# Kernel tuning notes

Hardware: AMD Instinct MI355X
Metric: run time of the kernel (lower is better)

## Reference

```python
import jax, jax.numpy as jnp
import numpy as np

N, E, D, H, C, G = 80000, 1280000, 64, 64, 5, 512


def setup_inputs() -> dict:
    key = jax.random.key(0)
    ks = jax.random.split(key, 8)
    h = jax.random.normal(ks[0], (N, D), jnp.float32)
    src = jax.random.randint(ks[1], (E,), 0, N)
    dst = jax.random.randint(ks[2], (E,), 0, N)
    graph_ids = jnp.sort(jax.random.randint(ks[3], (N,), 0, G))
    # Glorot-ish init for weights
    W1 = jax.random.normal(ks[4], (D, H), jnp.float32) * (1.0 / np.sqrt(D))
    b1 = jnp.zeros((H,), jnp.float32)
    W2 = jax.random.normal(ks[5], (H, H), jnp.float32) * (1.0 / np.sqrt(H))
    b2 = jnp.zeros((H,), jnp.float32)
    Wc = jax.random.normal(ks[6], (H, C), jnp.float32) * (1.0 / np.sqrt(H))
    bc = jnp.zeros((C,), jnp.float32)
    return dict(h=h, src=src, dst=dst, graph_ids=graph_ids,
                W1=W1, b1=b1, W2=W2, b2=b2, Wc=Wc, bc=bc, num_graphs=G)


def reference(h, src, dst, graph_ids, W1, b1, W2, b2, Wc, bc, num_graphs):
    n = h.shape[0]
    ones_e = jnp.ones(src.shape[0], h.dtype)
    # DGL GraphConv norm='both': symmetric normalization, degrees clamped to >=1
    out_deg = jnp.clip(jax.ops.segment_sum(ones_e, src, num_segments=n), 1.0)
    in_deg = jnp.clip(jax.ops.segment_sum(ones_e, dst, num_segments=n), 1.0)
    norm_src = jax.lax.rsqrt(out_deg)  # [N]
    norm_dst = jax.lax.rsqrt(in_deg)   # [N]

    def graph_conv(x, W, b):
        x = x * norm_src[:, None]                                   # scale by D_out^{-1/2}
        agg = jax.ops.segment_sum(x[src], dst, num_segments=n)      # sparse A^T x (copy_u + sum)
        agg = agg * norm_dst[:, None]                               # scale by D_in^{-1/2}
        return agg @ W + b

    h1 = jax.nn.relu(graph_conv(h, W1, b1))
    h2 = jax.nn.relu(graph_conv(h1, W2, b2))

    # dgl.mean_nodes: per-graph mean pooling over nodes
    cnt = jnp.clip(jax.ops.segment_sum(jnp.ones(n, h.dtype), graph_ids,
                                       num_segments=num_graphs), 1.0)
    hg = jax.ops.segment_sum(h2, graph_ids, num_segments=num_graphs) / cnt[:, None]
    return hg @ Wc + bc  # [G, C] logits
```

## Files before the change

kernel.cpp:

```cpp
#include <hip/hip_runtime.h>
#include <hip/hip_bf16.h>


#define NBK 160
#define HB  256
#define CAP 9216

typedef __attribute__((ext_vector_type(8))) short bf16x8;
typedef __attribute__((ext_vector_type(4))) float f32x4;

__device__ __forceinline__ float bflo(unsigned u) { return __uint_as_float(u << 16); }
__device__ __forceinline__ float bfhi(unsigned u) { return __uint_as_float(u & 0xffff0000u); }
__device__ __forceinline__ float bf1(unsigned short u) { return __uint_as_float((unsigned)u << 16); }
__device__ __forceinline__ unsigned short f2bf(float f) {
    unsigned u = __float_as_uint(f);
    return (unsigned short)((u + 0x7fff + ((u >> 16) & 1)) >> 16);
}
__device__ __forceinline__ unsigned packbf(float lo, float hi) {
    return (unsigned)f2bf(lo) | ((unsigned)f2bf(hi) << 16);
}

__global__ __launch_bounds__(256) void pA_scatter(
    const int* __restrict__ src, const int* __restrict__ dst,
    int* __restrict__ curD, int* __restrict__ curS,
    int* __restrict__ pack, unsigned short* __restrict__ sloc,
    const int* __restrict__ gids, int* __restrict__ goffs,
    int E, int NB, int N, int G)
{
    if (blockIdx.x >= HB) {
        int i = (blockIdx.x - HB) * 256 + threadIdx.x;
        if (i >= N) return;
        int b = gids[i];
        if (i == 0) {
            for (int g = 0; g <= b; g++) goffs[g] = 0;
        } else {
            int a = gids[i - 1];
            for (int g = a + 1; g <= b; g++) goffs[g] = i;
        }
        if (i == N - 1) {
            for (int g = b + 1; g <= G; g++) goffs[g] = N;
        }
        return;
    }
    __shared__ int hd[NBK], hs[NBK];
    int t = threadIdx.x;
    for (int i = t; i < NB; i += 256) { hd[i] = 0; hs[i] = 0; }
    __syncthreads();
    int chunk = (E + HB - 1) / HB;
    int s0 = blockIdx.x * chunk, s1 = min(E, s0 + chunk);
    int q0 = s0 >> 2, q1 = s1 >> 2;
    const int4* s4 = (const int4*)src;
    const int4* d4 = (const int4*)dst;
    for (int q = q0 + t; q < q1; q += 256) {
        int4 d = d4[q];
        int4 s = s4[q];
        atomicAdd(&hd[d.x >> 9], 1); atomicAdd(&hd[d.y >> 9], 1);
        atomicAdd(&hd[d.z >> 9], 1); atomicAdd(&hd[d.w >> 9], 1);
        atomicAdd(&hs[s.x >> 9], 1); atomicAdd(&hs[s.y >> 9], 1);
        atomicAdd(&hs[s.z >> 9], 1); atomicAdd(&hs[s.w >> 9], 1);
    }
    for (int i = (q1 << 2) + t; i < s1; i += 256) {
        atomicAdd(&hd[dst[i] >> 9], 1);
        atomicAdd(&hs[src[i] >> 9], 1);
    }
    __syncthreads();
    for (int b = t; b < NB; b += 256) {
        int cd = hd[b], cs = hs[b];
        hd[b] = cd ? atomicAdd(&curD[b], cd) : 0;
        hs[b] = cs ? atomicAdd(&curS[b], cs) : 0;
    }
    __syncthreads();
    for (int q = q0 + t; q < q1; q += 256) {
        int4 d = d4[q];
        int4 s = s4[q];
        #pragma unroll
        for (int j = 0; j < 4; j++) {
            int ss = j == 0 ? s.x : j == 1 ? s.y : j == 2 ? s.z : s.w;
            int dd = j == 0 ? d.x : j == 1 ? d.y : j == 2 ? d.z : d.w;
            int bd = dd >> 9, bs = ss >> 9;
            int pd = atomicAdd(&hd[bd], 1);
            int ps = atomicAdd(&hs[bs], 1);
            if (pd < CAP) pack[(size_t)bd * CAP + pd] = ((dd & 511) << 17) | ss;
            if (ps < CAP) sloc[(size_t)bs * CAP + ps] = (unsigned short)(ss & 511);
        }
    }
    for (int i = (q1 << 2) + t; i < s1; i += 256) {
        int s = src[i], d = dst[i];
        int bd = d >> 9, bs = s >> 9;
        int pd = atomicAdd(&hd[bd], 1);
        int ps = atomicAdd(&hs[bs], 1);
        if (pd < CAP) pack[(size_t)bd * CAP + pd] = ((d & 511) << 17) | s;
        if (ps < CAP) sloc[(size_t)bs * CAP + ps] = (unsigned short)(s & 511);
    }
}

__global__ __launch_bounds__(256) void p5_build(
    const int* __restrict__ pack, const unsigned short* __restrict__ sloc,
    const int* __restrict__ curD, const int* __restrict__ curS,
    int* __restrict__ col, int* __restrict__ row_offs, int* __restrict__ deg,
    float* __restrict__ nsrc, float* __restrict__ ndst,
    const float* __restrict__ h, unsigned short* __restrict__ xs,
    int N, int NB)
{
    __shared__ int hist[512];
    __shared__ float nsl[512];
    __shared__ int wt[4];
    int t = threadIdx.x;
    bool dmode = blockIdx.x < NB;
    int b = dmode ? blockIdx.x : blockIdx.x - NB;
    int n0 = b << 9, n1 = min(N, n0 + 512);
    hist[t] = 0; hist[t + 256] = 0;
    __syncthreads();
    int e0 = b * CAP;
    int tot = min(dmode ? curD[b] : curS[b], CAP);
    int e1 = e0 + tot;
    if (!dmode) {
        for (int i = e0 + t; i < e1; i += 256)
            atomicAdd(&hist[sloc[i]], 1);
        __syncthreads();
        for (int n = n0 + t; n < n1; n += 256) {
            float s = rsqrtf((float)max(hist[n - n0], 1));
            nsrc[n] = s;
            nsl[n - n0] = s;
        }
        __syncthreads();
        int cnt = n1 - n0;
        const float2* h2p = (const float2*)h;
        ushort2* xp = (ushort2*)xs;
        for (int i = t; i < cnt * 32; i += 256) {
            int node = i >> 5;
            float s = nsl[node];
            float2 v = h2p[(size_t)(n0 + node) * 32 + (i & 31)];
            ushort2 o;
            o.x = f2bf(v.x * s);
            o.y = f2bf(v.y * s);
            xp[(size_t)(n0 + node) * 32 + (i & 31)] = o;
        }
        return;
    }
    for (int i = e0 + t; i < e1; i += 256)
        atomicAdd(&hist[pack[i] >> 17], 1);
    __syncthreads();
    int c0 = hist[2 * t], c1 = hist[2 * t + 1];
    int v = c0 + c1;
    int lane = t & 63, w = t >> 6;
    int x = v;
    #pragma unroll
    for (int off = 1; off < 64; off <<= 1) {
        int y = __shfl_up(x, off);
        if (lane >= off) x += y;
    }
    if (lane == 63) wt[w] = x;
    __syncthreads();
    int bw = 0;
    for (int i = 0; i < w; i++) bw += wt[i];
    int excl = x - v + bw;
    int n = n0 + 2 * t;
    if (n < n1) {
        row_offs[n] = e0 + excl;
        deg[n] = c0;
        ndst[n] = rsqrtf((float)max(c0, 1));
    }
    if (n + 1 < n1) {
        row_offs[n + 1] = e0 + excl + c0;
        deg[n + 1] = c1;
        ndst[n + 1] = rsqrtf((float)max(c1, 1));
    }
    hist[2 * t] = excl;
    hist[2 * t + 1] = excl + c0;
    __syncthreads();
    for (int i = e0 + t; i < e1; i += 256) {
        int wd = pack[i];
        int pos = atomicAdd(&hist[wd >> 17], 1);
        col[e0 + pos] = wd & 0x1FFFF;
    }
}

__global__ __launch_bounds__(256) void agg_kernel(
    const unsigned short* __restrict__ z, unsigned short* __restrict__ y,
    const int* __restrict__ col, const int* __restrict__ row_offs,
    const int* __restrict__ deg, int N)
{
    int lane = threadIdx.x & 63;
    int sub  = lane >> 3;
    int li   = lane & 7;
    const uint4* x4 = (const uint4*)z;

    int wid = (blockIdx.x * 256 + threadIdx.x) >> 6;
    int nw  = (gridDim.x * 256) >> 6;

    int ro = 0, cnt = 0, idx = 0;
    if (wid < N) {
        ro = row_offs[wid];
        cnt = deg[wid];
        if (lane < min(cnt, 64)) idx = col[ro + lane];
    }
    for (int node = wid; node < N; node += nw) {
        int nnode = node + nw;
        int nro = 0, ncnt = 0;
        if (nnode < N) { nro = row_offs[nnode]; ncnt = deg[nnode]; }

        float a0=0.f,a1=0.f,a2=0.f,a3=0.f,a4=0.f,a5=0.f,a6=0.f,a7=0.f;
        int cc = 0;
        int cidx = idx;
        while (cc < cnt) {
            int m = min(cnt - cc, 64);
            for (int i = 0; i < m; i += 32) {
                int e1 = i + sub, e2 = i + 8 + sub, e3 = i + 16 + sub, e4 = i + 24 + sub;
                int s1 = __shfl(cidx, min(e1, m - 1));
                int s2 = __shfl(cidx, min(e2, m - 1));
                int s3 = __shfl(cidx, min(e3, m - 1));
                int s4 = __shfl(cidx, min(e4, m - 1));
                uint4 v1 = make_uint4(0u,0u,0u,0u), v2 = v1, v3 = v1, v4 = v1;
                if (e1 < m) v1 = x4[(size_t)s1 * 8 + li];
                if (e2 < m) v2 = x4[(size_t)s2 * 8 + li];
                if (e3 < m) v3 = x4[(size_t)s3 * 8 + li];
                if (e4 < m) v4 = x4[(size_t)s4 * 8 + li];
                a0 += bflo(v1.x); a1 += bfhi(v1.x);
                a2 += bflo(v1.y); a3 += bfhi(v1.y);
                a4 += bflo(v1.z); a5 += bfhi(v1.z);
                a6 += bflo(v1.w); a7 += bfhi(v1.w);
                a0 += bflo(v2.x); a1 += bfhi(v2.x);
                a2 += bflo(v2.y); a3 += bfhi(v2.y);
                a4 += bflo(v2.z); a5 += bfhi(v2.z);
                a6 += bflo(v2.w); a7 += bfhi(v2.w);
                a0 += bflo(v3.x); a1 += bfhi(v3.x);
                a2 += bflo(v3.y); a3 += bfhi(v3.y);
                a4 += bflo(v3.z); a5 += bfhi(v3.z);
                a6 += bflo(v3.w); a7 += bfhi(v3.w);
                a0 += bflo(v4.x); a1 += bfhi(v4.x);
                a2 += bflo(v4.y); a3 += bfhi(v4.y);
                a4 += bflo(v4.z); a5 += bfhi(v4.z);
                a6 += bflo(v4.w); a7 += bfhi(v4.w);
            }
            cc += 64;
            if (cc < cnt) cidx = (lane < min(cnt - cc, 64)) ? col[ro + cc + lane] : 0;
        }
        idx = 0;
        if (nnode < N && lane < min(ncnt, 64)) idx = col[nro + lane];

        #pragma unroll
        for (int off = 8; off <= 32; off <<= 1) {
            a0 += __shfl_xor(a0, off); a1 += __shfl_xor(a1, off);
            a2 += __shfl_xor(a2, off); a3 += __shfl_xor(a3, off);
            a4 += __shfl_xor(a4, off); a5 += __shfl_xor(a5, off);
            a6 += __shfl_xor(a6, off); a7 += __shfl_xor(a7, off);
        }
        if (sub == 0) {
            uint4 o;
            o.x = packbf(a0, a1);
            o.y = packbf(a2, a3);
            o.z = packbf(a4, a5);
            o.w = packbf(a6, a7);
            ((uint4*)y)[(size_t)node * 8 + li] = o;
        }
        ro = nro; cnt = ncnt;
    }
}

__global__ __launch_bounds__(256) void gemm_kernel(
    const unsigned short* __restrict__ A, const float* __restrict__ W,
    const float* __restrict__ b, const float* __restrict__ ndst,
    const float* __restrict__ nsrc, unsigned short* __restrict__ Z,
    int M, int scale_out)
{
    int t = threadIdx.x, lane = t & 63, w = t >> 6;
    int col = lane & 15, quad = lane >> 4;
    bf16x8 bfrag[4][2];
    #pragma unroll
    for (int nt = 0; nt < 4; nt++)
        #pragma unroll
        for (int ks = 0; ks < 2; ks++)
            #pragma unroll
            for (int j = 0; j < 8; j++)
                bfrag[nt][ks][j] =
                    (short)f2bf(W[(ks * 32 + quad * 8 + j) * 64 + nt * 16 + col]);
    float bias[4];
    #pragma unroll
    for (int nt = 0; nt < 4; nt++) bias[nt] = b[nt * 16 + col];

    int mbase = blockIdx.x * 64 + w * 16;
    if (mbase >= M) return;
    int row = min(mbase + col, M - 1);
    const uint4* a4 = (const uint4*)A;
    union { uint4 u; bf16x8 v; } a0, a1;
    a0.u = a4[(size_t)row * 8 + quad];
    a1.u = a4[(size_t)row * 8 + 4 + quad];

    float nd[4], ns[4];
    #pragma unroll
    for (int r = 0; r < 4; r++) {
        int m = min(mbase + quad * 4 + r, M - 1);
        nd[r] = ndst[m];
        ns[r] = scale_out ? nsrc[m] : 1.f;
    }

    #pragma unroll
    for (int nt = 0; nt < 4; nt++) {
        f32x4 acc = {0.f, 0.f, 0.f, 0.f};
        acc = __builtin_amdgcn_mfma_f32_16x16x32_bf16(a0.v, bfrag[nt][0], acc, 0, 0, 0);
        acc = __builtin_amdgcn_mfma_f32_16x16x32_bf16(a1.v, bfrag[nt][1], acc, 0, 0, 0);
        #pragma unroll
        for (int r = 0; r < 4; r++) {
            int m = mbase + quad * 4 + r;
            if (m < M)
                Z[(size_t)m * 64 + nt * 16 + col] =
                    f2bf(fmaxf(nd[r] * acc[r] + bias[nt], 0.f) * ns[r]);
        }
    }
}

__global__ __launch_bounds__(256) void pool_kernel(
    const unsigned short* __restrict__ h2, const int* __restrict__ goffs,
    const float* __restrict__ Wc, const float* __restrict__ bc,
    float* __restrict__ out)
{
    int g = blockIdx.x;
    int lane = threadIdx.x & 63;
    int w = threadIdx.x >> 6;
    int s = goffs[g], e = goffs[g + 1];
    float acc = 0.f;
    for (int i = s + w; i < e; i += 4) acc += bf1(h2[i * 64 + lane]);
    __shared__ float red[4][64];
    red[w][lane] = acc;
    __syncthreads();
    if (w == 0) {
        float tot = red[0][lane] + red[1][lane] + red[2][lane] + red[3][lane];
        float mean = tot / (float)max(e - s, 1);
        float wc[5];
        #pragma unroll
        for (int c = 0; c < 5; c++) wc[c] = Wc[lane * 5 + c];
        #pragma unroll
        for (int c = 0; c < 5; c++) {
            float p = mean * wc[c];
            #pragma unroll
            for (int off = 32; off; off >>= 1) p += __shfl_down(p, off);
            if (lane == 0) out[g * 5 + c] = p + bc[c];
        }
    }
}

extern "C" void kernel_launch(void* const* d_in, const int* in_sizes, int n_in,
                              void* d_out, int out_size, void* d_ws, size_t ws_size,
                              hipStream_t stream)
{
    const float* h    = (const float*)d_in[0];
    const int*   src  = (const int*)d_in[1];
    const int*   dst  = (const int*)d_in[2];
    const int*   gids = (const int*)d_in[3];
    const float* W1   = (const float*)d_in[4];
    const float* b1   = (const float*)d_in[5];
    const float* W2   = (const float*)d_in[6];
    const float* b2   = (const float*)d_in[7];
    const float* Wc   = (const float*)d_in[8];
    const float* bc   = (const float*)d_in[9];
    float* out = (float*)d_out;

    const int N = in_sizes[0] / 64;
    const int E = in_sizes[1];
    const int G = out_size / 5;
    const int NB = (N + 511) >> 9;
    const int NBB = (N + 255) / 256;

    auto align = [](size_t x) { return (x + 255) & ~(size_t)255; };
    char* p = (char*)d_ws;
    int* curD    = (int*)p;            p += align((size_t)2 * NBK * 4);
    int* curS    = curD + NBK;
    int* row_offs= (int*)p;            p += align((size_t)N * 4);
    int* deg     = (int*)p;            p += align((size_t)N * 4);
    float* nsrc  = (float*)p;          p += align((size_t)N * 4);
    float* ndst  = (float*)p;          p += align((size_t)N * 4);
    int* goffs   = (int*)p;            p += align((size_t)(G + 1) * 4);
    int* pack    = (int*)p;            p += align((size_t)NBK * CAP * 4);
    unsigned short* sloc = (unsigned short*)p; p += align((size_t)NBK * CAP * 2);
    int* col     = (int*)p;            p += align((size_t)NBK * CAP * 4);
    unsigned short* xs  = (unsigned short*)p; p += align((size_t)N * 64 * 2);
    unsigned short* s1  = (unsigned short*)p; p += align((size_t)N * 64 * 2);
    unsigned short* h1s = (unsigned short*)p; p += align((size_t)N * 64 * 2);
    unsigned short* s2  = s1;
    unsigned short* h2  = xs;

    hipMemsetAsync(curD, 0, (size_t)2 * NBK * 4, stream);

    pA_scatter<<<HB + NBB, 256, 0, stream>>>(src, dst, curD, curS, pack, sloc,
                                             gids, goffs, E, NB, N, G);
    p5_build<<<2 * NB, 256, 0, stream>>>(pack, sloc, curD, curS, col,
                                         row_offs, deg, nsrc, ndst, h, xs, N, NB);

    agg_kernel<<<4096, 256, 0, stream>>>(xs, s1, col, row_offs, deg, N);
    gemm_kernel<<<(N + 63) / 64, 256, 0, stream>>>(s1, W1, b1, ndst, nsrc,
                                                   h1s, N, 1);
    agg_kernel<<<4096, 256, 0, stream>>>(h1s, s2, col, row_offs, deg, N);
    gemm_kernel<<<(N + 63) / 64, 256, 0, stream>>>(s2, W2, b2, ndst, nsrc,
                                                   h2, N, 0);

    pool_kernel<<<G, 256, 0, stream>>>(h2, goffs, Wc, bc, out);
}
```

Measured before the change: 224.4 us.

## Fuse all seven kernels into one cooperative persistent kernel with grid syncs

Replaces the sequence of scatter, CSR build, two aggregation, two GEMM and pooling launches with a single cooperative kernel. The phases are separated by grid-wide syncs and use grid-stride loops over virtual blocks. This removes per-launch overhead and inter-kernel gaps. In exchange the grid is capped at the occupancy limit, which may reduce parallelism for agg (previously 4096 blocks) and adds grid-barrier cost.

```diff
diff --git a/kernel.cpp b/kernel.cpp
--- a/kernel.cpp
+++ b/kernel.cpp
@@ -1,5 +1,8 @@
 #include <hip/hip_runtime.h>
 #include <hip/hip_bf16.h>
+#include <hip/hip_cooperative_groups.h>
+
+namespace cg = cooperative_groups;
 
 
 #define NBK 160
@@ -20,171 +23,15 @@
     return (unsigned)f2bf(lo) | ((unsigned)f2bf(hi) << 16);
 }
 
-__global__ __launch_bounds__(256) void pA_scatter(
-    const int* __restrict__ src, const int* __restrict__ dst,
-    int* __restrict__ curD, int* __restrict__ curS,
-    int* __restrict__ pack, unsigned short* __restrict__ sloc,
-    const int* __restrict__ gids, int* __restrict__ goffs,
-    int E, int NB, int N, int G)
-{
-    if (blockIdx.x >= HB) {
-        int i = (blockIdx.x - HB) * 256 + threadIdx.x;
-        if (i >= N) return;
-        int b = gids[i];
-        if (i == 0) {
-            for (int g = 0; g <= b; g++) goffs[g] = 0;
-        } else {
-            int a = gids[i - 1];
-            for (int g = a + 1; g <= b; g++) goffs[g] = i;
-        }
-        if (i == N - 1) {
-            for (int g = b + 1; g <= G; g++) goffs[g] = N;
-        }
-        return;
-    }
-    __shared__ int hd[NBK], hs[NBK];
-    int t = threadIdx.x;
-    for (int i = t; i < NB; i += 256) { hd[i] = 0; hs[i] = 0; }
-    __syncthreads();
-    int chunk = (E + HB - 1) / HB;
-    int s0 = blockIdx.x * chunk, s1 = min(E, s0 + chunk);
-    int q0 = s0 >> 2, q1 = s1 >> 2;
-    const int4* s4 = (const int4*)src;
-    const int4* d4 = (const int4*)dst;
-    for (int q = q0 + t; q < q1; q += 256) {
-        int4 d = d4[q];
-        int4 s = s4[q];
-        atomicAdd(&hd[d.x >> 9], 1); atomicAdd(&hd[d.y >> 9], 1);
-        atomicAdd(&hd[d.z >> 9], 1); atomicAdd(&hd[d.w >> 9], 1);
-        atomicAdd(&hs[s.x >> 9], 1); atomicAdd(&hs[s.y >> 9], 1);
-        atomicAdd(&hs[s.z >> 9], 1); atomicAdd(&hs[s.w >> 9], 1);
-    }
-    for (int i = (q1 << 2) + t; i < s1; i += 256) {
-        atomicAdd(&hd[dst[i] >> 9], 1);
-        atomicAdd(&hs[src[i] >> 9], 1);
-    }
-    __syncthreads();
-    for (int b = t; b < NB; b += 256) {
-        int cd = hd[b], cs = hs[b];
-        hd[b] = cd ? atomicAdd(&curD[b], cd) : 0;
-        hs[b] = cs ? atomicAdd(&curS[b], cs) : 0;
-    }
-    __syncthreads();
-    for (int q = q0 + t; q < q1; q += 256) {
-        int4 d = d4[q];
-        int4 s = s4[q];
-        #pragma unroll
-        for (int j = 0; j < 4; j++) {
-            int ss = j == 0 ? s.x : j == 1 ? s.y : j == 2 ? s.z : s.w;
-            int dd = j == 0 ? d.x : j == 1 ? d.y : j == 2 ? d.z : d.w;
-            int bd = dd >> 9, bs = ss >> 9;
-            int pd = atomicAdd(&hd[bd], 1);
-            int ps = atomicAdd(&hs[bs], 1);
-            if (pd < CAP) pack[(size_t)bd * CAP + pd] = ((dd & 511) << 17) | ss;
-            if (ps < CAP) sloc[(size_t)bs * CAP + ps] = (unsigned short)(ss & 511);
-        }
-    }
-    for (int i = (q1 << 2) + t; i < s1; i += 256) {
-        int s = src[i], d = dst[i];
-        int bd = d >> 9, bs = s >> 9;
-        int pd = atomicAdd(&hd[bd], 1);
-        int ps = atomicAdd(&hs[bs], 1);
-        if (pd < CAP) pack[(size_t)bd * CAP + pd] = ((d & 511) << 17) | s;
-        if (ps < CAP) sloc[(size_t)bs * CAP + ps] = (unsigned short)(s & 511);
-    }
-}
-
-__global__ __launch_bounds__(256) void p5_build(
-    const int* __restrict__ pack, const unsigned short* __restrict__ sloc,
-    const int* __restrict__ curD, const int* __restrict__ curS,
-    int* __restrict__ col, int* __restrict__ row_offs, int* __restrict__ deg,
-    float* __restrict__ nsrc, float* __restrict__ ndst,
-    const float* __restrict__ h, unsigned short* __restrict__ xs,
-    int N, int NB)
-{
-    __shared__ int hist[512];
-    __shared__ float nsl[512];
-    __shared__ int wt[4];
-    int t = threadIdx.x;
-    bool dmode = blockIdx.x < NB;
-    int b = dmode ? blockIdx.x : blockIdx.x - NB;
-    int n0 = b << 9, n1 = min(N, n0 + 512);
-    hist[t] = 0; hist[t + 256] = 0;
-    __syncthreads();
-    int e0 = b * CAP;
-    int tot = min(dmode ? curD[b] : curS[b], CAP);
-    int e1 = e0 + tot;
-    if (!dmode) {
-        for (int i = e0 + t; i < e1; i += 256)
-            atomicAdd(&hist[sloc[i]], 1);
-        __syncthreads();
-        for (int n = n0 + t; n < n1; n += 256) {
-            float s = rsqrtf((float)max(hist[n - n0], 1));
-            nsrc[n] = s;
-            nsl[n - n0] = s;
-        }
-        __syncthreads();
-        int cnt = n1 - n0;
-        const float2* h2p = (const float2*)h;
-        ushort2* xp = (ushort2*)xs;
-        for (int i = t; i < cnt * 32; i += 256) {
-            int node = i >> 5;
-            float s = nsl[node];
-            float2 v = h2p[(size_t)(n0 + node) * 32 + (i & 31)];
-            ushort2 o;
-            o.x = f2bf(v.x * s);
-            o.y = f2bf(v.y * s);
-            xp[(size_t)(n0 + node) * 32 + (i & 31)] = o;
-        }
-        return;
-    }
-    for (int i = e0 + t; i < e1; i += 256)
-        atomicAdd(&hist[pack[i] >> 17], 1);
-    __syncthreads();
-    int c0 = hist[2 * t], c1 = hist[2 * t + 1];
-    int v = c0 + c1;
-    int lane = t & 63, w = t >> 6;
-    int x = v;
-    #pragma unroll
-    for (int off = 1; off < 64; off <<= 1) {
-        int y = __shfl_up(x, off);
-        if (lane >= off) x += y;
-    }
-    if (lane == 63) wt[w] = x;
-    __syncthreads();
-    int bw = 0;
-    for (int i = 0; i < w; i++) bw += wt[i];
-    int excl = x - v + bw;
-    int n = n0 + 2 * t;
-    if (n < n1) {
-        row_offs[n] = e0 + excl;
-        deg[n] = c0;
-        ndst[n] = rsqrtf((float)max(c0, 1));
-    }
-    if (n + 1 < n1) {
-        row_offs[n + 1] = e0 + excl + c0;
-        deg[n + 1] = c1;
-        ndst[n + 1] = rsqrtf((float)max(c1, 1));
-    }
-    hist[2 * t] = excl;
-    hist[2 * t + 1] = excl + c0;
-    __syncthreads();
-    for (int i = e0 + t; i < e1; i += 256) {
-        int wd = pack[i];
-        int pos = atomicAdd(&hist[wd >> 17], 1);
-        col[e0 + pos] = wd & 0x1FFFF;
-    }
-}
-
-__global__ __launch_bounds__(256) void agg_kernel(
-    const unsigned short* __restrict__ z, unsigned short* __restrict__ y,
-    const int* __restrict__ col, const int* __restrict__ row_offs,
+__device__ __forceinline__ void agg_body(
+    const unsigned short* __restrict__ zin, unsigned short* __restrict__ yout,
+    const int* __restrict__ cols, const int* __restrict__ row_offs,
     const int* __restrict__ deg, int N)
 {
     int lane = threadIdx.x & 63;
     int sub  = lane >> 3;
     int li   = lane & 7;
-    const uint4* x4 = (const uint4*)z;
+    const uint4* x4 = (const uint4*)zin;
 
     int wid = (blockIdx.x * 256 + threadIdx.x) >> 6;
     int nw  = (gridDim.x * 256) >> 6;
@@ -193,7 +40,7 @@
     if (wid < N) {
         ro = row_offs[wid];
         cnt = deg[wid];
-        if (lane < min(cnt, 64)) idx = col[ro + lane];
+        if (lane < min(cnt, 64)) idx = cols[ro + lane];
     }
     for (int node = wid; node < N; node += nw) {
         int nnode = node + nw;
@@ -234,10 +81,10 @@
                 a6 += bflo(v4.w); a7 += bfhi(v4.w);
             }
             cc += 64;
-            if (cc < cnt) cidx = (lane < min(cnt - cc, 64)) ? col[ro + cc + lane] : 0;
+            if (cc < cnt) cidx = (lane < min(cnt - cc, 64)) ? cols[ro + cc + lane] : 0;
         }
         idx = 0;
-        if (nnode < N && lane < min(ncnt, 64)) idx = col[nro + lane];
+        if (nnode < N && lane < min(ncnt, 64)) idx = cols[nro + lane];
 
         #pragma unroll
         for (int off = 8; off <= 32; off <<= 1) {
@@ -252,20 +99,20 @@
             o.y = packbf(a2, a3);
             o.z = packbf(a4, a5);
             o.w = packbf(a6, a7);
-            ((uint4*)y)[(size_t)node * 8 + li] = o;
+            ((uint4*)yout)[(size_t)node * 8 + li] = o;
         }
         ro = nro; cnt = ncnt;
     }
 }
 
-__global__ __launch_bounds__(256) void gemm_kernel(
+__device__ __forceinline__ void gemm_body(
     const unsigned short* __restrict__ A, const float* __restrict__ W,
-    const float* __restrict__ b, const float* __restrict__ ndst,
+    const float* __restrict__ bb, const float* __restrict__ ndst,
     const float* __restrict__ nsrc, unsigned short* __restrict__ Z,
     int M, int scale_out)
 {
-    int t = threadIdx.x, lane = t & 63, w = t >> 6;
-    int col = lane & 15, quad = lane >> 4;
+    int t = threadIdx.x, lane = t & 63, w4 = t >> 6;
+    int cl = lane & 15, quad = lane >> 4;
     bf16x8 bfrag[4][2];
     #pragma unroll
     for (int nt = 0; nt < 4; nt++)
@@ -274,69 +121,246 @@
             #pragma unroll
             for (int j = 0; j < 8; j++)
                 bfrag[nt][ks][j] =
-                    (short)f2bf(W[(ks * 32 + quad * 8 + j) * 64 + nt * 16 + col]);
+                    (short)f2bf(W[(ks * 32 + quad * 8 + j) * 64 + nt * 16 + cl]);
     float bias[4];
     #pragma unroll
-    for (int nt = 0; nt < 4; nt++) bias[nt] = b[nt * 16 + col];
-
-    int mbase = blockIdx.x * 64 + w * 16;
-    if (mbase >= M) return;
-    int row = min(mbase + col, M - 1);
-    const uint4* a4 = (const uint4*)A;
-    union { uint4 u; bf16x8 v; } a0, a1;
-    a0.u = a4[(size_t)row * 8 + quad];
-    a1.u = a4[(size_t)row * 8 + 4 + quad];
-
-    float nd[4], ns[4];
-    #pragma unroll
-    for (int r = 0; r < 4; r++) {
-        int m = min(mbase + quad * 4 + r, M - 1);
-        nd[r] = ndst[m];
-        ns[r] = scale_out ? nsrc[m] : 1.f;
-    }
-
-    #pragma unroll
-    for (int nt = 0; nt < 4; nt++) {
-        f32x4 acc = {0.f, 0.f, 0.f, 0.f};
-        acc = __builtin_amdgcn_mfma_f32_16x16x32_bf16(a0.v, bfrag[nt][0], acc, 0, 0, 0);
-        acc = __builtin_amdgcn_mfma_f32_16x16x32_bf16(a1.v, bfrag[nt][1], acc, 0, 0, 0);
+    for (int nt = 0; nt < 4; nt++) bias[nt] = bb[nt * 16 + cl];
+
+    int ntiles = (M + 63) >> 6;
+    for (int tb = blockIdx.x; tb < ntiles; tb += gridDim.x) {
+        int mbase = tb * 64 + w4 * 16;
+        if (mbase >= M) continue;
+        int row = min(mbase + cl, M - 1);
+        const uint4* a4 = (const uint4*)A;
+        union { uint4 u; bf16x8 v; } a0, a1;
+        a0.u = a4[(size_t)row * 8 + quad];
+        a1.u = a4[(size_t)row * 8 + 4 + quad];
+
+        float nd[4], ns[4];
         #pragma unroll
         for (int r = 0; r < 4; r++) {
-            int m = mbase + quad * 4 + r;
-            if (m < M)
-                Z[(size_t)m * 64 + nt * 16 + col] =
-                    f2bf(fmaxf(nd[r] * acc[r] + bias[nt], 0.f) * ns[r]);
-        }
-    }
-}
-
-__global__ __launch_bounds__(256) void pool_kernel(
-    const unsigned short* __restrict__ h2, const int* __restrict__ goffs,
+            int m = min(mbase + quad * 4 + r, M - 1);
+            nd[r] = ndst[m];
+            ns[r] = scale_out ? nsrc[m] : 1.f;
+        }
+
+        #pragma unroll
+        for (int nt = 0; nt < 4; nt++) {
+            f32x4 acc = {0.f, 0.f, 0.f, 0.f};
+            acc = __builtin_amdgcn_mfma_f32_16x16x32_bf16(a0.v, bfrag[nt][0], acc, 0, 0, 0);
+            acc = __builtin_amdgcn_mfma_f32_16x16x32_bf16(a1.v, bfrag[nt][1], acc, 0, 0, 0);
+            #pragma unroll
+            for (int r = 0; r < 4; r++) {
+                int m = mbase + quad * 4 + r;
+                if (m < M)
+                    Z[(size_t)m * 64 + nt * 16 + cl] =
+                        f2bf(fmaxf(nd[r] * acc[r] + bias[nt], 0.f) * ns[r]);
+            }
+        }
+    }
+}
+
+__global__ __launch_bounds__(256, 4) void fused_all(
+    const float* __restrict__ h, const int* __restrict__ src,
+    const int* __restrict__ dst, const int* __restrict__ gids,
+    const float* __restrict__ W1, const float* __restrict__ b1,
+    const float* __restrict__ W2, const float* __restrict__ b2,
     const float* __restrict__ Wc, const float* __restrict__ bc,
-    float* __restrict__ out)
+    float* __restrict__ out,
+    int* curD, int* curS, int* row_offs, int* deg,
+    float* nsrc, float* ndst, int* goffs, int* pack,
+    unsigned short* sloc, int* cols,
+    unsigned short* xs, unsigned short* sb1, unsigned short* h1s,
+    int N, int E, int G, int NB)
 {
-    int g = blockIdx.x;
-    int lane = threadIdx.x & 63;
-    int w = threadIdx.x >> 6;
-    int s = goffs[g], e = goffs[g + 1];
-    float acc = 0.f;
-    for (int i = s + w; i < e; i += 4) acc += bf1(h2[i * 64 + lane]);
-    __shared__ float red[4][64];
-    red[w][lane] = acc;
-    __syncthreads();
-    if (w == 0) {
-        float tot = red[0][lane] + red[1][lane] + red[2][lane] + red[3][lane];
-        float mean = tot / (float)max(e - s, 1);
-        float wc[5];
-        #pragma unroll
-        for (int c = 0; c < 5; c++) wc[c] = Wc[lane * 5 + c];
-        #pragma unroll
-        for (int c = 0; c < 5; c++) {
-            float p = mean * wc[c];
+    cg::grid_group gg = cg::this_grid();
+    __shared__ int smem[1040];
+    const int t = threadIdx.x;
+    const int NBB = (N + 255) >> 8;
+
+    for (int vb = blockIdx.x; vb < HB + NBB; vb += gridDim.x) {
+        if (vb >= HB) {
+            int i = (vb - HB) * 256 + t;
+            if (i < N) {
+                int b = gids[i];
+                if (i == 0) {
+                    for (int g = 0; g <= b; g++) goffs[g] = 0;
+                } else {
+                    int a = gids[i - 1];
+                    for (int g = a + 1; g <= b; g++) goffs[g] = i;
+                }
+                if (i == N - 1) {
+                    for (int g = b + 1; g <= G; g++) goffs[g] = N;
+                }
+            }
+        } else {
+            int* hd = smem;
+            int* hs = smem + NBK;
+            for (int i = t; i < NB; i += 256) { hd[i] = 0; hs[i] = 0; }
+            __syncthreads();
+            int chunk = (E + HB - 1) / HB;
+            int s0 = vb * chunk, se = min(E, s0 + chunk);
+            int q0 = s0 >> 2, q1 = se >> 2;
+            const int4* s4 = (const int4*)src;
+            const int4* d4 = (const int4*)dst;
+            for (int q = q0 + t; q < q1; q += 256) {
+                int4 d = d4[q];
+                int4 s = s4[q];
+                atomicAdd(&hd[d.x >> 9], 1); atomicAdd(&hd[d.y >> 9], 1);
+                atomicAdd(&hd[d.z >> 9], 1); atomicAdd(&hd[d.w >> 9], 1);
+                atomicAdd(&hs[s.x >> 9], 1); atomicAdd(&hs[s.y >> 9], 1);
+                atomicAdd(&hs[s.z >> 9], 1); atomicAdd(&hs[s.w >> 9], 1);
+            }
+            for (int i = (q1 << 2) + t; i < se; i += 256) {
+                atomicAdd(&hd[dst[i] >> 9], 1);
+                atomicAdd(&hs[src[i] >> 9], 1);
+            }
+            __syncthreads();
+            for (int b = t; b < NB; b += 256) {
+                int cd = hd[b], cs = hs[b];
+                hd[b] = cd ? atomicAdd(&curD[b], cd) : 0;
+                hs[b] = cs ? atomicAdd(&curS[b], cs) : 0;
+            }
+            __syncthreads();
+            for (int q = q0 + t; q < q1; q += 256) {
+                int4 d = d4[q];
+                int4 s = s4[q];
+                #pragma unroll
+                for (int j = 0; j < 4; j++) {
+                    int ss = j == 0 ? s.x : j == 1 ? s.y : j == 2 ? s.z : s.w;
+                    int dd = j == 0 ? d.x : j == 1 ? d.y : j == 2 ? d.z : d.w;
+                    int bd = dd >> 9, bs = ss >> 9;
+                    int pd = atomicAdd(&hd[bd], 1);
+                    int ps = atomicAdd(&hs[bs], 1);
+                    if (pd < CAP) pack[(size_t)bd * CAP + pd] = ((dd & 511) << 17) | ss;
+                    if (ps < CAP) sloc[(size_t)bs * CAP + ps] = (unsigned short)(ss & 511);
+                }
+            }
+            for (int i = (q1 << 2) + t; i < se; i += 256) {
+                int s = src[i], d = dst[i];
+                int bd = d >> 9, bs = s >> 9;
+                int pd = atomicAdd(&hd[bd], 1);
+                int ps = atomicAdd(&hs[bs], 1);
+                if (pd < CAP) pack[(size_t)bd * CAP + pd] = ((d & 511) << 17) | s;
+                if (ps < CAP) sloc[(size_t)bs * CAP + ps] = (unsigned short)(s & 511);
+            }
+            __syncthreads();
+        }
+    }
+    gg.sync();
+
+    for (int vb = blockIdx.x; vb < 2 * NB; vb += gridDim.x) {
+        int* hist = smem;
+        float* nsl = (float*)(smem + 512);
+        int* wt = smem + 1024;
+        bool dmode = vb < NB;
+        int b = dmode ? vb : vb - NB;
+        int n0 = b << 9, n1 = min(N, n0 + 512);
+        hist[t] = 0; hist[t + 256] = 0;
+        __syncthreads();
+        int e0 = b * CAP;
+        int tot = min(dmode ? curD[b] : curS[b], CAP);
+        int e1 = e0 + tot;
+        if (!dmode) {
+            for (int i = e0 + t; i < e1; i += 256)
+                atomicAdd(&hist[sloc[i]], 1);
+            __syncthreads();
+            for (int n = n0 + t; n < n1; n += 256) {
+                float sc = rsqrtf((float)max(hist[n - n0], 1));
+                nsrc[n] = sc;
+                nsl[n - n0] = sc;
+            }
+            __syncthreads();
+            int cnt = n1 - n0;
+            const float2* h2p = (const float2*)h;
+            ushort2* xp = (ushort2*)xs;
+            for (int i = t; i < cnt * 32; i += 256) {
+                int node = i >> 5;
+                float sc = nsl[node];
+                float2 v = h2p[(size_t)(n0 + node) * 32 + (i & 31)];
+                ushort2 o;
+                o.x = f2bf(v.x * sc);
+                o.y = f2bf(v.y * sc);
+                xp[(size_t)(n0 + node) * 32 + (i & 31)] = o;
+            }
+        } else {
+            for (int i = e0 + t; i < e1; i += 256)
+                atomicAdd(&hist[pack[i] >> 17], 1);
+            __syncthreads();
+            int c0 = hist[2 * t], c1 = hist[2 * t + 1];
+            int v = c0 + c1;
+            int lane = t & 63, w4 = t >> 6;
+            int x = v;
             #pragma unroll
-            for (int off = 32; off; off >>= 1) p += __shfl_down(p, off);
-            if (lane == 0) out[g * 5 + c] = p + bc[c];
-        }
+            for (int off = 1; off < 64; off <<= 1) {
+                int y = __shfl_up(x, off);
+                if (lane >= off) x += y;
+            }
+            if (lane == 63) wt[w4] = x;
+            __syncthreads();
+            int bw = 0;
+            for (int i = 0; i < w4; i++) bw += wt[i];
+            int excl = x - v + bw;
+            int n = n0 + 2 * t;
+            if (n < n1) {
+                row_offs[n] = e0 + excl;
+                deg[n] = c0;
+                ndst[n] = rsqrtf((float)max(c0, 1));
+            }
+            if (n + 1 < n1) {
+                row_offs[n + 1] = e0 + excl + c0;
+                deg[n + 1] = c1;
+                ndst[n + 1] = rsqrtf((float)max(c1, 1));
+            }
+            hist[2 * t] = excl;
+            hist[2 * t + 1] = excl + c0;
+            __syncthreads();
+            for (int i = e0 + t; i < e1; i += 256) {
+                int wd = pack[i];
+                int pos = atomicAdd(&hist[wd >> 17], 1);
+                cols[e0 + pos] = wd & 0x1FFFF;
+            }
+        }
+        __syncthreads();
+    }
+    gg.sync();
+
+    agg_body(xs, sb1, cols, row_offs, deg, N);
+    gg.sync();
+    gemm_body(sb1, W1, b1, ndst, nsrc, h1s, N, 1);
+    gg.sync();
+
+    agg_body(h1s, sb1, cols, row_offs, deg, N);
+    gg.sync();
+    gemm_body(sb1, W2, b2, ndst, nsrc, xs, N, 0);
+    gg.sync();
+
+    const unsigned short* h2 = xs;
+    for (int g = blockIdx.x; g < G; g += gridDim.x) {
+        int lane = t & 63;
+        int w4 = t >> 6;
+        int s = goffs[g], e = goffs[g + 1];
+        float acc = 0.f;
+        for (int i = s + w4; i < e; i += 4) acc += bf1(h2[(size_t)i * 64 + lane]);
+        float* red = (float*)smem;
+        red[w4 * 64 + lane] = acc;
+        __syncthreads();
+        if (w4 == 0) {
+            float tot = red[0 * 64 + lane] + red[1 * 64 + lane] +
+                        red[2 * 64 + lane] + red[3 * 64 + lane];
+            float mean = tot / (float)max(e - s, 1);
+            float wc[5];
+            #pragma unroll
+            for (int c = 0; c < 5; c++) wc[c] = Wc[lane * 5 + c];
+            #pragma unroll
+            for (int c = 0; c < 5; c++) {
+                float p = mean * wc[c];
+                #pragma unroll
+                for (int off = 32; off; off >>= 1) p += __shfl_down(p, off);
+                if (lane == 0) out[g * 5 + c] = p + bc[c];
+            }
+        }
+        __syncthreads();
     }
 }
 
@@ -356,11 +380,10 @@
     const float* bc   = (const float*)d_in[9];
     float* out = (float*)d_out;
 
-    const int N = in_sizes[0] / 64;
-    const int E = in_sizes[1];
-    const int G = out_size / 5;
-    const int NB = (N + 511) >> 9;
-    const int NBB = (N + 255) / 256;
+    int N = in_sizes[0] / 64;
+    int E = in_sizes[1];
+    int G = out_size / 5;
+    int NB = (N + 511) >> 9;
 
     auto align = [](size_t x) { return (x + 255) & ~(size_t)255; };
     char* p = (char*)d_ws;
@@ -373,26 +396,26 @@
     int* goffs   = (int*)p;            p += align((size_t)(G + 1) * 4);
     int* pack    = (int*)p;            p += align((size_t)NBK * CAP * 4);
     unsigned short* sloc = (unsigned short*)p; p += align((size_t)NBK * CAP * 2);
-    int* col     = (int*)p;            p += align((size_t)NBK * CAP * 4);
+    int* cols    = (int*)p;            p += align((size_t)NBK * CAP * 4);
     unsigned short* xs  = (unsigned short*)p; p += align((size_t)N * 64 * 2);
-    unsigned short* s1  = (unsigned short*)p; p += align((size_t)N * 64 * 2);
+    unsigned short* sb1 = (unsigned short*)p; p += align((size_t)N * 64 * 2);
     unsigned short* h1s = (unsigned short*)p; p += align((size_t)N * 64 * 2);
-    unsigned short* s2  = s1;
-    unsigned short* h2  = xs;
+
+    static int grid_blocks = 0;
+    if (grid_blocks == 0) {
+        int perCU = 0;
+        if (hipOccupancyMaxActiveBlocksPerMultiprocessor(&perCU, fused_all, 256, 0)
+                != hipSuccess || perCU < 1)
+            perCU = 2;
+        grid_blocks = perCU * 256;
+        if (grid_blocks > 2048) grid_blocks = 2048;
+    }
 
     hipMemsetAsync(curD, 0, (size_t)2 * NBK * 4, stream);
 
-    pA_scatter<<<HB + NBB, 256, 0, stream>>>(src, dst, curD, curS, pack, sloc,
-                                             gids, goffs, E, NB, N, G);
-    p5_build<<<2 * NB, 256, 0, stream>>>(pack, sloc, curD, curS, col,
-                                         row_offs, deg, nsrc, ndst, h, xs, N, NB);
-
-    agg_kernel<<<4096, 256, 0, stream>>>(xs, s1, col, row_offs, deg, N);
-    gemm_kernel<<<(N + 63) / 64, 256, 0, stream>>>(s1, W1, b1, ndst, nsrc,
-                                                   h1s, N, 1);
-    agg_kernel<<<4096, 256, 0, stream>>>(h1s, s2, col, row_offs, deg, N);
-    gemm_kernel<<<(N + 63) / 64, 256, 0, stream>>>(s2, W2, b2, ndst, nsrc,
-                                                   h2, N, 0);
-
-    pool_kernel<<<G, 256, 0, stream>>>(h2, goffs, Wc, bc, out);
-}
+    void* args[] = { &h, &src, &dst, &gids, &W1, &b1, &W2, &b2, &Wc, &bc, &out,
+                     &curD, &curS, &row_offs, &deg, &nsrc, &ndst, &goffs, &pack,
+                     &sloc, &cols, &xs, &sb1, &h1s, &N, &E, &G, &NB };
+    hipLaunchCooperativeKernel((void*)fused_all, dim3(grid_blocks), dim3(256),
+                               args, 0, stream);
+}
```

Measured after the change: 655.4 us. 2.92x slower.

## Fuse aggregation with dense transform and pooling into per-node GEMV kernels

Applied to the files above, without the earlier changes.

Each layer's aggregation kernel now multiplies the aggregated row by the weight matrix directly, using a per-wave scalar GEMV with W kept in shared memory, instead of writing an intermediate and running a separate MFMA GEMM kernel. The second layer accumulates its output straight into per-graph sums with atomics, which removes the h2 write and the pool read. The goal is to drop two kernel launches and the intermediate activation traffic. The cost is 64 FMAs plus 64 shuffles per node on CUDA cores instead of MFMA, a 16KB shared-memory load of W per block, and float atomic contention on graph accumulators.

```diff
diff --git a/kernel.cpp b/kernel.cpp
--- a/kernel.cpp
+++ b/kernel.cpp
@@ -15,9 +15,6 @@
 __device__ __forceinline__ unsigned short f2bf(float f) {
     unsigned u = __float_as_uint(f);
     return (unsigned short)((u + 0x7fff + ((u >> 16) & 1)) >> 16);
-}
-__device__ __forceinline__ unsigned packbf(float lo, float hi) {
-    return (unsigned)f2bf(lo) | ((unsigned)f2bf(hi) << 16);
 }
 
 __global__ __launch_bounds__(256) void pA_scatter(
@@ -176,15 +173,24 @@
     }
 }
 
-__global__ __launch_bounds__(256) void agg_kernel(
-    const unsigned short* __restrict__ z, unsigned short* __restrict__ y,
-    const int* __restrict__ col, const int* __restrict__ row_offs,
-    const int* __restrict__ deg, int N)
-{
+template<int MODE>
+__global__ __launch_bounds__(256) void agg_gemv(
+    const unsigned short* __restrict__ zin, unsigned short* __restrict__ yout,
+    const int* __restrict__ cols, const int* __restrict__ row_offs,
+    const int* __restrict__ deg, const float* __restrict__ W,
+    const float* __restrict__ bias, const float* __restrict__ ndst,
+    const float* __restrict__ nsrc, const int* __restrict__ gids,
+    float* __restrict__ gacc, int N)
+{
+    __shared__ float Wl[4096];
+    for (int i = threadIdx.x; i < 4096; i += 256) Wl[i] = W[i];
+    __syncthreads();
+
     int lane = threadIdx.x & 63;
     int sub  = lane >> 3;
     int li   = lane & 7;
-    const uint4* x4 = (const uint4*)z;
+    float bv = bias[lane];
+    const uint4* x4 = (const uint4*)zin;
 
     int wid = (blockIdx.x * 256 + threadIdx.x) >> 6;
     int nw  = (gridDim.x * 256) >> 6;
@@ -193,14 +199,14 @@
     if (wid < N) {
         ro = row_offs[wid];
         cnt = deg[wid];
-        if (lane < min(cnt, 64)) idx = col[ro + lane];
+        if (lane < min(cnt, 64)) idx = cols[ro + lane];
     }
     for (int node = wid; node < N; node += nw) {
         int nnode = node + nw;
         int nro = 0, ncnt = 0;
         if (nnode < N) { nro = row_offs[nnode]; ncnt = deg[nnode]; }
 
-        float a0=0.f,a1=0.f,a2=0.f,a3=0.f,a4=0.f,a5=0.f,a6=0.f,a7=0.f;
+        float av[8] = {0.f,0.f,0.f,0.f,0.f,0.f,0.f,0.f};
         int cc = 0;
         int cidx = idx;
         while (cc < cnt) {
@@ -216,127 +222,73 @@
                 if (e2 < m) v2 = x4[(size_t)s2 * 8 + li];
                 if (e3 < m) v3 = x4[(size_t)s3 * 8 + li];
                 if (e4 < m) v4 = x4[(size_t)s4 * 8 + li];
-                a0 += bflo(v1.x); a1 += bfhi(v1.x);
-                a2 += bflo(v1.y); a3 += bfhi(v1.y);
-                a4 += bflo(v1.z); a5 += bfhi(v1.z);
-                a6 += bflo(v1.w); a7 += bfhi(v1.w);
-                a0 += bflo(v2.x); a1 += bfhi(v2.x);
-                a2 += bflo(v2.y); a3 += bfhi(v2.y);
-                a4 += bflo(v2.z); a5 += bfhi(v2.z);
-                a6 += bflo(v2.w); a7 += bfhi(v2.w);
-                a0 += bflo(v3.x); a1 += bfhi(v3.x);
-                a2 += bflo(v3.y); a3 += bfhi(v3.y);
-                a4 += bflo(v3.z); a5 += bfhi(v3.z);
-                a6 += bflo(v3.w); a7 += bfhi(v3.w);
-                a0 += bflo(v4.x); a1 += bfhi(v4.x);
-                a2 += bflo(v4.y); a3 += bfhi(v4.y);
-                a4 += bflo(v4.z); a5 += bfhi(v4.z);
-                a6 += bflo(v4.w); a7 += bfhi(v4.w);
+                av[0] += bflo(v1.x); av[1] += bfhi(v1.x);
+                av[2] += bflo(v1.y); av[3] += bfhi(v1.y);
+                av[4] += bflo(v1.z); av[5] += bfhi(v1.z);
+                av[6] += bflo(v1.w); av[7] += bfhi(v1.w);
+                av[0] += bflo(v2.x); av[1] += bfhi(v2.x);
+                av[2] += bflo(v2.y); av[3] += bfhi(v2.y);
+                av[4] += bflo(v2.z); av[5] += bfhi(v2.z);
+                av[6] += bflo(v2.w); av[7] += bfhi(v2.w);
+                av[0] += bflo(v3.x); av[1] += bfhi(v3.x);
+                av[2] += bflo(v3.y); av[3] += bfhi(v3.y);
+                av[4] += bflo(v3.z); av[5] += bfhi(v3.z);
+                av[6] += bflo(v3.w); av[7] += bfhi(v3.w);
+                av[0] += bflo(v4.x); av[1] += bfhi(v4.x);
+                av[2] += bflo(v4.y); av[3] += bfhi(v4.y);
+                av[4] += bflo(v4.z); av[5] += bfhi(v4.z);
+                av[6] += bflo(v4.w); av[7] += bfhi(v4.w);
             }
             cc += 64;
-            if (cc < cnt) cidx = (lane < min(cnt - cc, 64)) ? col[ro + cc + lane] : 0;
+            if (cc < cnt) cidx = (lane < min(cnt - cc, 64)) ? cols[ro + cc + lane] : 0;
         }
         idx = 0;
-        if (nnode < N && lane < min(ncnt, 64)) idx = col[nro + lane];
+        if (nnode < N && lane < min(ncnt, 64)) idx = cols[nro + lane];
 
         #pragma unroll
         for (int off = 8; off <= 32; off <<= 1) {
-            a0 += __shfl_xor(a0, off); a1 += __shfl_xor(a1, off);
-            a2 += __shfl_xor(a2, off); a3 += __shfl_xor(a3, off);
-            a4 += __shfl_xor(a4, off); a5 += __shfl_xor(a5, off);
-            a6 += __shfl_xor(a6, off); a7 += __shfl_xor(a7, off);
-        }
-        if (sub == 0) {
-            uint4 o;
-            o.x = packbf(a0, a1);
-            o.y = packbf(a2, a3);
-            o.z = packbf(a4, a5);
-            o.w = packbf(a6, a7);
-            ((uint4*)y)[(size_t)node * 8 + li] = o;
+            #pragma unroll
+            for (int r = 0; r < 8; r++) av[r] += __shfl_xor(av[r], off);
+        }
+        float zv = 0.f;
+        for (int kb = 0; kb < 8; kb++) {
+            #pragma unroll
+            for (int r = 0; r < 8; r++) {
+                float sk = __shfl(av[r], kb);
+                zv += sk * Wl[(kb * 8 + r) * 64 + lane];
+            }
+        }
+        float nd = ndst[node];
+        zv = fmaxf(nd * zv + bv, 0.f);
+        if (MODE == 0) {
+            zv *= nsrc[node];
+            int u = (int)f2bf(zv);
+            int o = u | (__shfl_down(u, 1) << 16);
+            if (!(lane & 1))
+                ((unsigned*)yout)[(size_t)node * 32 + (lane >> 1)] = (unsigned)o;
+        } else {
+            int g = gids[node];
+            atomicAdd(&gacc[(size_t)g * 64 + lane], zv);
         }
         ro = nro; cnt = ncnt;
     }
 }
 
-__global__ __launch_bounds__(256) void gemm_kernel(
-    const unsigned short* __restrict__ A, const float* __restrict__ W,
-    const float* __restrict__ b, const float* __restrict__ ndst,
-    const float* __restrict__ nsrc, unsigned short* __restrict__ Z,
-    int M, int scale_out)
-{
-    int t = threadIdx.x, lane = t & 63, w = t >> 6;
-    int col = lane & 15, quad = lane >> 4;
-    bf16x8 bfrag[4][2];
+__global__ __launch_bounds__(64) void cls_kernel(
+    const float* __restrict__ gacc, const int* __restrict__ goffs,
+    const float* __restrict__ Wc, const float* __restrict__ bc,
+    float* __restrict__ out, int G)
+{
+    int g = blockIdx.x;
+    int lane = threadIdx.x;
+    float cnt = (float)max(goffs[g + 1] - goffs[g], 1);
+    float mean = gacc[(size_t)g * 64 + lane] / cnt;
     #pragma unroll
-    for (int nt = 0; nt < 4; nt++)
+    for (int c = 0; c < 5; c++) {
+        float p = mean * Wc[lane * 5 + c];
         #pragma unroll
-        for (int ks = 0; ks < 2; ks++)
-            #pragma unroll
-            for (int j = 0; j < 8; j++)
-                bfrag[nt][ks][j] =
-                    (short)f2bf(W[(ks * 32 + quad * 8 + j) * 64 + nt * 16 + col]);
-    float bias[4];
-    #pragma unroll
-    for (int nt = 0; nt < 4; nt++) bias[nt] = b[nt * 16 + col];
-
-    int mbase = blockIdx.x * 64 + w * 16;
-    if (mbase >= M) return;
-    int row = min(mbase + col, M - 1);
-    const uint4* a4 = (const uint4*)A;
-    union { uint4 u; bf16x8 v; } a0, a1;
-    a0.u = a4[(size_t)row * 8 + quad];
-    a1.u = a4[(size_t)row * 8 + 4 + quad];
-
-    float nd[4], ns[4];
-    #pragma unroll
-    for (int r = 0; r < 4; r++) {
-        int m = min(mbase + quad * 4 + r, M - 1);
-        nd[r] = ndst[m];
-        ns[r] = scale_out ? nsrc[m] : 1.f;
-    }
-
-    #pragma unroll
-    for (int nt = 0; nt < 4; nt++) {
-        f32x4 acc = {0.f, 0.f, 0.f, 0.f};
-        acc = __builtin_amdgcn_mfma_f32_16x16x32_bf16(a0.v, bfrag[nt][0], acc, 0, 0, 0);
-        acc = __builtin_amdgcn_mfma_f32_16x16x32_bf16(a1.v, bfrag[nt][1], acc, 0, 0, 0);
-        #pragma unroll
-        for (int r = 0; r < 4; r++) {
-            int m = mbase + quad * 4 + r;
-            if (m < M)
-                Z[(size_t)m * 64 + nt * 16 + col] =
-                    f2bf(fmaxf(nd[r] * acc[r] + bias[nt], 0.f) * ns[r]);
-        }
-    }
-}
-
-__global__ __launch_bounds__(256) void pool_kernel(
-    const unsigned short* __restrict__ h2, const int* __restrict__ goffs,
-    const float* __restrict__ Wc, const float* __restrict__ bc,
-    float* __restrict__ out)
-{
-    int g = blockIdx.x;
-    int lane = threadIdx.x & 63;
-    int w = threadIdx.x >> 6;
-    int s = goffs[g], e = goffs[g + 1];
-    float acc = 0.f;
-    for (int i = s + w; i < e; i += 4) acc += bf1(h2[i * 64 + lane]);
-    __shared__ float red[4][64];
-    red[w][lane] = acc;
-    __syncthreads();
-    if (w == 0) {
-        float tot = red[0][lane] + red[1][lane] + red[2][lane] + red[3][lane];
-        float mean = tot / (float)max(e - s, 1);
-        float wc[5];
-        #pragma unroll
-        for (int c = 0; c < 5; c++) wc[c] = Wc[lane * 5 + c];
-        #pragma unroll
-        for (int c = 0; c < 5; c++) {
-            float p = mean * wc[c];
-            #pragma unroll
-            for (int off = 32; off; off >>= 1) p += __shfl_down(p, off);
-            if (lane == 0) out[g * 5 + c] = p + bc[c];
-        }
+        for (int off = 32; off; off >>= 1) p += __shfl_down(p, off);
+        if (lane == 0) out[g * 5 + c] = p + bc[c];
     }
 }
 
@@ -364,8 +316,11 @@
 
     auto align = [](size_t x) { return (x + 255) & ~(size_t)255; };
     char* p = (char*)d_ws;
-    int* curD    = (int*)p;            p += align((size_t)2 * NBK * 4);
+    int* curD    = (int*)p;
     int* curS    = curD + NBK;
+    float* gacc  = (float*)(p + (size_t)2 * NBK * 4);
+    size_t zbytes = (size_t)2 * NBK * 4 + (size_t)G * 64 * 4;
+    p += align(zbytes);
     int* row_offs= (int*)p;            p += align((size_t)N * 4);
     int* deg     = (int*)p;            p += align((size_t)N * 4);
     float* nsrc  = (float*)p;          p += align((size_t)N * 4);
@@ -373,26 +328,20 @@
     int* goffs   = (int*)p;            p += align((size_t)(G + 1) * 4);
     int* pack    = (int*)p;            p += align((size_t)NBK * CAP * 4);
     unsigned short* sloc = (unsigned short*)p; p += align((size_t)NBK * CAP * 2);
-    int* col     = (int*)p;            p += align((size_t)NBK * CAP * 4);
+    int* cols    = (int*)p;            p += align((size_t)NBK * CAP * 4);
     unsigned short* xs  = (unsigned short*)p; p += align((size_t)N * 64 * 2);
-    unsigned short* s1  = (unsigned short*)p; p += align((size_t)N * 64 * 2);
     unsigned short* h1s = (unsigned short*)p; p += align((size_t)N * 64 * 2);
-    unsigned short* s2  = s1;
-    unsigned short* h2  = xs;
-
-    hipMemsetAsync(curD, 0, (size_t)2 * NBK * 4, stream);
+
+    hipMemsetAsync(curD, 0, zbytes, stream);
 
     pA_scatter<<<HB + NBB, 256, 0, stream>>>(src, dst, curD, curS, pack, sloc,
                                              gids, goffs, E, NB, N, G);
-    p5_build<<<2 * NB, 256, 0, stream>>>(pack, sloc, curD, curS, col,
+    p5_build<<<2 * NB, 256, 0, stream>>>(pack, sloc, curD, curS, cols,
                                          row_offs, deg, nsrc, ndst, h, xs, N, NB);
 
-    agg_kernel<<<4096, 256, 0, stream>>>(xs, s1, col, row_offs, deg, N);
-    gemm_kernel<<<(N + 63) / 64, 256, 0, stream>>>(s1, W1, b1, ndst, nsrc,
-                                                   h1s, N, 1);
-    agg_kernel<<<4096, 256, 0, stream>>>(h1s, s2, col, row_offs, deg, N);
-    gemm_kernel<<<(N + 63) / 64, 256, 0, stream>>>(s2, W2, b2, ndst, nsrc,
-                                                   h2, N, 0);
-
-    pool_kernel<<<G, 256, 0, stream>>>(h2, goffs, Wc, bc, out);
-}
+    agg_gemv<0><<<4096, 256, 0, stream>>>(xs, h1s, cols, row_offs, deg,
+                                          W1, b1, ndst, nsrc, nullptr, nullptr, N);
+    agg_gemv<1><<<4096, 256, 0, stream>>>(h1s, nullptr, cols, row_offs, deg,
+                                          W2, b2, ndst, nullptr, gids, gacc, N);
+    cls_kernel<<<G, 64, 0, stream>>>(gacc, goffs, Wc, bc, out, G);
+}
```

New measurement: 337.8 us. 1.51x slower.
